# Kernel optimization log

Hardware: AMD Instinct MI355X
Metric: run time of the kernel (lower is better)

## Reference

```python
import jax, jax.numpy as jnp
import numpy as np
from functools import partial

DIM = 256
HEADS = 8
HEAD_DIM = DIM // HEADS
SCALES = (1, 2, 4)
B, H, W = 1, 64, 64


def _dwconv3x3(x, w, b):
    # x: (B,C,H,W), w: (C,1,3,3) depthwise, b: (C,)
    y = jax.lax.conv_general_dilated(
        x, w, window_strides=(1, 1), padding='SAME',
        feature_group_count=x.shape[1],
        dimension_numbers=('NCHW', 'OIHW', 'NCHW'))
    return y + b[None, :, None, None]


def _pwconv(x, w, b):
    # 1x1 conv: x (B,C,H,W), w (O,C), b (O,)
    return jnp.einsum('bchw,oc->bohw', x, w) + b[None, :, None, None]


def _avg_pool(x, s):
    Bb, C, Hh, Ww = x.shape
    return x.reshape(Bb, C, Hh // s, s, Ww // s, s).mean(axis=(3, 5))


def setup_inputs() -> dict:
    key = jax.random.key(0)
    ks = jax.random.split(key, 9)
    sc = 0.05
    return {
        'x': jax.random.normal(ks[0], (B, DIM, H, W), dtype=jnp.float32),
        'dw_w': jax.random.normal(ks[1], (3, DIM, 1, 3, 3), dtype=jnp.float32) * sc,
        'dw_b': jax.random.normal(ks[2], (3, DIM), dtype=jnp.float32) * sc,
        'pw_w': jax.random.normal(ks[3], (3, 3 * DIM, DIM), dtype=jnp.float32) * sc,
        'pw_b': jax.random.normal(ks[4], (3, 3 * DIM), dtype=jnp.float32) * sc,
        'pos_w': jax.random.normal(ks[5], (3, DIM, 1, 3, 3), dtype=jnp.float32) * sc,
        'pos_b': jax.random.normal(ks[6], (3, DIM), dtype=jnp.float32) * sc,
        'fusion_w': jax.random.normal(ks[7], (DIM, 3 * DIM), dtype=jnp.float32) * sc,
        'fusion_b': jax.random.normal(ks[8], (DIM,), dtype=jnp.float32) * sc,
    }


def reference(x, dw_w, dw_b, pw_w, pw_b, pos_w, pos_b, fusion_w, fusion_b):
    Bb, C, Hh, Ww = x.shape
    outputs = []
    for i, scale in enumerate(SCALES):
        xs = _avg_pool(x, scale) if scale > 1 else x
        # ConvQKV
        x_dw = _dwconv3x3(xs, dw_w[i], dw_b[i])
        qkv = _pwconv(x_dw, pw_w[i], pw_b[i])
        q, k, v = jnp.split(qkv, 3, axis=1)
        pos = _dwconv3x3(xs, pos_w[i], pos_b[i])
        q = q + pos
        k = k + pos
        Hs, Ws = xs.shape[2], xs.shape[3]
        Ns = Hs * Ws
        # (B, heads, head_dim, N)
        q = q.reshape(Bb, HEADS, HEAD_DIM, Ns)
        k = k.reshape(Bb, HEADS, HEAD_DIM, Ns)
        v = v.reshape(Bb, HEADS, HEAD_DIM, Ns)
        attn = jnp.einsum('bhdn,bhdm->bhnm', q, k) / (HEAD_DIM ** 0.5)
        attn = jax.nn.softmax(attn, axis=-1)
        out = jnp.einsum('bhnm,bhdm->bhdn', attn, v)  # (B,h,hd,N)
        out = out.reshape(Bb, C, Hs, Ws)
        if scale > 1:
            out = jax.image.resize(out, (Bb, C, Hh, Ww), method='bilinear')
        outputs.append(out)
    cat = jnp.concatenate(outputs, axis=1)  # (B, 3C, H, W)
    return jnp.einsum('bchw,oc->bohw', cat, fusion_w) + fusion_b[None, :, None, None]
```

## Files before the change

### kernel.cpp

```cpp
#include <hip/hip_runtime.h>
#include <math.h>

#define DIM 256
#define HEADS 8
#define HD 32
#define QSCALE 0.25504526770295183f

typedef __attribute__((ext_vector_type(8))) short bf16x8;
typedef __attribute__((ext_vector_type(4))) float f32x4;

#if __has_builtin(__builtin_amdgcn_exp2f)
#define EXP2(x) __builtin_amdgcn_exp2f(x)
#else
#define EXP2(x) __expf((x) * 0.6931471805599453f)
#endif

__device__ __forceinline__ unsigned short f2bf(float f) {
  unsigned int u = __float_as_uint(f);
  unsigned int r = u + 0x7fff + ((u >> 16) & 1);
  return (unsigned short)(r >> 16);
}
__device__ __forceinline__ float bf2f(unsigned short u) {
  return __uint_as_float(((unsigned int)u) << 16);
}


__global__ __launch_bounds__(256) void prep_kernel(const float* __restrict__ x,
    const float* __restrict__ pw_w, const float* __restrict__ fus_w,
    float* __restrict__ xs2, float* __restrict__ xs4,
    unsigned short* __restrict__ Wb, unsigned short* __restrict__ Wf) {
  const int gx = blockIdx.x, t = threadIdx.x;
  if (gx < 1024) {
    int id = gx * 256 + t;
    int c = id >> 10, n = id & 1023;
    int y = (n >> 5) << 1, x0 = (n & 31) << 1;
    const float* b = x + c * 4096 + y * 64 + x0;
    xs2[id] = (b[0] + b[1] + b[64] + b[65]) * 0.25f;
  } else if (gx < 1280) {
    int id = (gx - 1024) * 256 + t;
    int c = id >> 8, n = id & 255;
    int y = (n >> 4) << 2, x0 = (n & 15) << 2;
    const float* b = x + c * 4096 + y * 64 + x0;
    float s = 0.f;
    #pragma unroll
    for (int dy = 0; dy < 4; ++dy)
      #pragma unroll
      for (int dx = 0; dx < 4; ++dx) s += b[dy * 64 + dx];
    xs4[id] = s * 0.0625f;
  } else if (gx < 1424) {
    int lid = (gx - 1280) * 256 + t;
    int fb = lid >> 5, l = lid & 31;
    int scale = fb / 384, bs = fb - scale * 384;
    int rtile = bs >> 3, kchunk = bs & 7;
    int r = scale * 768 + rtile * 16 + (l & 7) * 2;
    int k = kchunk * 32 + (l >> 3) * 8;
    const float* s0 = pw_w + (size_t)r * 256 + k;
    float4 u0 = *(const float4*)(s0);
    float4 u1 = *(const float4*)(s0 + 4);
    float4 u2 = *(const float4*)(s0 + 256);
    float4 u3 = *(const float4*)(s0 + 260);
    unsigned short* d = Wb + (size_t)fb * 512 + l * 16;
    ushort4 a0 = {f2bf(u0.x), f2bf(u0.y), f2bf(u0.z), f2bf(u0.w)};
    ushort4 a1 = {f2bf(u1.x), f2bf(u1.y), f2bf(u1.z), f2bf(u1.w)};
    ushort4 a2 = {f2bf(u2.x), f2bf(u2.y), f2bf(u2.z), f2bf(u2.w)};
    ushort4 a3 = {f2bf(u3.x), f2bf(u3.y), f2bf(u3.z), f2bf(u3.w)};
    *(ushort4*)(d)      = a0;
    *(ushort4*)(d + 4)  = a1;
    *(ushort4*)(d + 8)  = a2;
    *(ushort4*)(d + 12) = a3;
  } else {
    int lid = (gx - 1424) * 256 + t;
    int fb = lid >> 5, l = lid & 31;
    int rtile = fb / 24, kchunk = fb - rtile * 24;
    int r = rtile * 16 + (l & 7) * 2;
    int k = kchunk * 32 + (l >> 3) * 8;
    const float* s0 = fus_w + (size_t)r * 768 + k;
    float4 u0 = *(const float4*)(s0);
    float4 u1 = *(const float4*)(s0 + 4);
    float4 u2 = *(const float4*)(s0 + 768);
    float4 u3 = *(const float4*)(s0 + 772);
    unsigned short* d = Wf + (size_t)fb * 512 + l * 16;
    ushort4 a0 = {f2bf(u0.x), f2bf(u0.y), f2bf(u0.z), f2bf(u0.w)};
    ushort4 a1 = {f2bf(u1.x), f2bf(u1.y), f2bf(u1.z), f2bf(u1.w)};
    ushort4 a2 = {f2bf(u2.x), f2bf(u2.y), f2bf(u2.z), f2bf(u2.w)};
    ushort4 a3 = {f2bf(u3.x), f2bf(u3.y), f2bf(u3.z), f2bf(u3.w)};
    *(ushort4*)(d)      = a0;
    *(ushort4*)(d + 4)  = a1;
    *(ushort4*)(d + 8)  = a2;
    *(ushort4*)(d + 12) = a3;
  }
}

__global__ __launch_bounds__(256) void dwt_kernel(const float* __restrict__ x,
    const float* __restrict__ xs2, const float* __restrict__ xs4,
    const float* __restrict__ dw_w, const float* __restrict__ dw_b,
    const float* __restrict__ pos_w, const float* __restrict__ pos_b,
    unsigned short* __restrict__ xdwT, unsigned short* __restrict__ posT) {
  __shared__ unsigned short lds1[32][72];
  __shared__ unsigned short lds2[32][72];
  int b = blockIdx.x;
  const float* src;
  int lgHs, wo, soff;
  if (b < 512)      { src = x;   lgHs = 6; wo = 0; soff = 0; }
  else if (b < 640) { b -= 512; src = xs2; lgHs = 5; wo = 1; soff = 1048576; }
  else              { b -= 640; src = xs4; lgHs = 4; wo = 2; soff = 1310720; }
  const int c0 = (b & 3) * 64;
  const int n0 = (b >> 2) * 32;
  const int Hs = 1 << lgHs;
  const int Ns = Hs * Hs;
  const int t = threadIdx.x;
  #pragma unroll
  for (int p = 0; p < 2; ++p) {
    int cl = p * 32 + (t >> 3);
    int c = c0 + cl;
    const float* w1 = dw_w + wo * 2304 + c * 9;
    const float* w2 = pos_w + wo * 2304 + c * 9;
    float b1 = dw_b[wo * 256 + c], b2 = pos_b[wo * 256 + c];
    int nb = (t & 7) * 4;
    int gn = n0 + nb;
    int y = gn >> lgHs, xg = gn & (Hs - 1);
    const float* sc = src + c * Ns;
    float r[3][6];
    #pragma unroll
    for (int ky = 0; ky < 3; ++ky) {
      int yy = y + ky - 1;
      bool rok = (yy >= 0) && (yy < Hs);
      #pragma unroll
      for (int j = 0; j < 6; ++j) {
        int xx = xg - 1 + j;
        r[ky][j] = (rok && xx >= 0 && xx < Hs) ? sc[yy * Hs + xx] : 0.f;
      }
    }
    #pragma unroll
    for (int i = 0; i < 4; ++i) {
      float s1 = b1, s2 = b2;
      #pragma unroll
      for (int ky = 0; ky < 3; ++ky)
        #pragma unroll
        for (int kx = 0; kx < 3; ++kx) {
          float v = r[ky][i + kx];
          s1 += v * w1[ky * 3 + kx];
          s2 += v * w2[ky * 3 + kx];
        }
      lds1[nb + i][cl] = f2bf(s1);
      lds2[nb + i][cl] = f2bf(s2);
    }
  }
  __syncthreads();
  {
    int blk = t >> 6, l = t & 63;
    int ntile = blk >> 1, cchunk = blk & 1;
    int koct = l >> 4, rr = l & 15;
    size_t bid = (size_t)((n0 >> 4) + ntile) * 8 + (c0 >> 5) + cchunk;
    *(bf16x8*)(xdwT + soff + bid * 512 + (size_t)l * 8) =
        *(const bf16x8*)&lds1[ntile * 16 + rr][cchunk * 32 + koct * 8];
  }
  {
    int n = t >> 3, cseg = (t & 7) * 8;
    *(bf16x8*)(posT + soff + (size_t)(n0 + n) * 256 + c0 + cseg) =
        *(const bf16x8*)&lds2[n][cseg];
  }
}

__global__ __launch_bounds__(256) void gemm_qkv_all(const unsigned short* __restrict__ WbA,
    const unsigned short* __restrict__ xdwTA, const float* __restrict__ biasA,
    const unsigned short* __restrict__ posTA, unsigned short* __restrict__ Qf,
    unsigned short* __restrict__ Kf, unsigned short* __restrict__ Vf) {
  int by = blockIdx.y;
  int Ns, off;
  const unsigned short *Wb, *xdwT, *posT;
  const float* bias;
  if (by < 64) {
    Ns = 4096; off = 0;
    Wb = WbA; bias = biasA;
  } else if (by < 80) {
    Ns = 1024; off = 1048576; by -= 64;
    Wb = WbA + 196608; bias = biasA + 768;
  } else {
    Ns = 256; off = 1310720; by -= 80;
    Wb = WbA + 393216; bias = biasA + 1536;
  }
  xdwT = xdwTA + off; posT = posTA + off;
  const int t = threadIdx.x;
  const int wave = t >> 6, lane = t & 63;
  const int ln = lane & 15, quad = lane >> 4;
  const int o0 = blockIdx.x * 64 + (wave & 1) * 32;
  const int n0 = by * 64 + (wave >> 1) * 32;
  const int at0 = (o0 >> 4) * 8, at1 = at0 + 8;
  const int bt0 = (n0 >> 4) * 8, bt1 = bt0 + 8;
  const bool vblk = blockIdx.x >= 8;
  f32x4 acc[2][2] = {};
  if (!vblk) {
    #pragma unroll
    for (int ks = 0; ks < 8; ++ks) {
      bf16x8 af0 = *(const bf16x8*)(Wb + (size_t)(at0 + ks) * 512 + lane * 8);
      bf16x8 af1 = *(const bf16x8*)(Wb + (size_t)(at1 + ks) * 512 + lane * 8);
      bf16x8 bv0 = *(const bf16x8*)(xdwT + (size_t)(bt0 + ks) * 512 + lane * 8);
      bf16x8 bv1 = *(const bf16x8*)(xdwT + (size_t)(bt1 + ks) * 512 + lane * 8);
      acc[0][0] = __builtin_amdgcn_mfma_f32_16x16x32_bf16(af0, bv0, acc[0][0], 0, 0, 0);
      acc[0][1] = __builtin_amdgcn_mfma_f32_16x16x32_bf16(af0, bv1, acc[0][1], 0, 0, 0);
      acc[1][0] = __builtin_amdgcn_mfma_f32_16x16x32_bf16(af1, bv0, acc[1][0], 0, 0, 0);
      acc[1][1] = __builtin_amdgcn_mfma_f32_16x16x32_bf16(af1, bv1, acc[1][1], 0, 0, 0);
    }
  } else {
    #pragma unroll
    for (int ks = 0; ks < 8; ++ks) {
      bf16x8 af0 = *(const bf16x8*)(Wb + (size_t)(at0 + ks) * 512 + lane * 8);
      bf16x8 af1 = *(const bf16x8*)(Wb + (size_t)(at1 + ks) * 512 + lane * 8);
      bf16x8 bv0 = *(const bf16x8*)(xdwT + (size_t)(bt0 + ks) * 512 + lane * 8);
      bf16x8 bv1 = *(const bf16x8*)(xdwT + (size_t)(bt1 + ks) * 512 + lane * 8);
      acc[0][0] = __builtin_amdgcn_mfma_f32_16x16x32_bf16(bv0, af0, acc[0][0], 0, 0, 0);
      acc[0][1] = __builtin_amdgcn_mfma_f32_16x16x32_bf16(bv0, af1, acc[0][1], 0, 0, 0);
      acc[1][0] = __builtin_amdgcn_mfma_f32_16x16x32_bf16(bv1, af0, acc[1][0], 0, 0, 0);
      acc[1][1] = __builtin_amdgcn_mfma_f32_16x16x32_bf16(bv1, af1, acc[1][1], 0, 0, 0);
    }
  }
  if (!vblk) {
    const int cat = blockIdx.x >> 2;
    #pragma unroll
    for (int mt = 0; mt < 2; ++mt) {
      int ot = o0 + mt * 16 + quad * 4;
      float bs0 = bias[ot], bs1 = bias[ot + 1], bs2 = bias[ot + 2], bs3 = bias[ot + 3];
      #pragma unroll
      for (int nt = 0; nt < 2; ++nt) {
        int nn = n0 + nt * 16 + ln;
        f32x4 v = acc[mt][nt];
        v.x += bs0; v.y += bs1; v.z += bs2; v.w += bs3;
        int c = ot & 255;
        ushort4 p4 = *(const ushort4*)(posT + (size_t)nn * 256 + c);
        v.x += bf2f(p4.x); v.y += bf2f(p4.y); v.z += bf2f(p4.z); v.w += bf2f(p4.w);
        if (cat == 0) { v.x *= QSCALE; v.y *= QSCALE; v.z *= QSCALE; v.w *= QSCALE; }
        ushort4 st;
        st.x = f2bf(v.x); st.y = f2bf(v.y); st.z = f2bf(v.z); st.w = f2bf(v.w);
        int hh = c >> 5, d = c & 31;
        unsigned short* dst = (cat == 0 ? Qf : Kf) + off;
        size_t a = ((size_t)(hh * (Ns >> 4) + (nn >> 4)) * 64 + (d >> 3) * 16 + (nn & 15)) * 8
                   + (d & 7);
        *(ushort4*)(dst + a) = st;
      }
    }
  } else {
    #pragma unroll
    for (int a = 0; a < 2; ++a) {
      int nbase = n0 + a * 16 + quad * 4;
      #pragma unroll
      for (int bb = 0; bb < 2; ++bb) {
        int o = o0 + bb * 16 + ln;
        int c = o - 512;
        int hh = c >> 5, d = c & 31;
        int dt = d >> 4, dl = d & 15;
        float bs = bias[o];
        f32x4 v = acc[a][bb];
        ushort4 st;
        st.x = f2bf(v.x + bs); st.y = f2bf(v.y + bs);
        st.z = f2bf(v.z + bs); st.w = f2bf(v.w + bs);
        size_t adr = ((((size_t)hh * (Ns >> 5) + (nbase >> 5)) * 2 + dt) * 64
                      + ((nbase & 31) >> 3) * 16 + dl) * 8 + (nbase & 7);
        *(ushort4*)(Vf + off + adr) = st;
      }
    }
  }
}

__global__ __launch_bounds__(256) void attn_all_kernel(
    const unsigned short* __restrict__ Qf, const unsigned short* __restrict__ Kf,
    const unsigned short* __restrict__ Vf,
    unsigned short* __restrict__ accp1, unsigned short* __restrict__ p2,
    unsigned short* __restrict__ p4, float* __restrict__ ls1,
    float* __restrict__ ls2, float* __restrict__ ls4) {
  __shared__ unsigned short pt_lds[4 * 32 * 72];
  const int z = blockIdx.z;
  unsigned short* accp;
  float* lsump;
  int Ns, lgMs, sp, off;
  if (z < 8) {
    accp = accp1; lsump = ls1; Ns = 4096; lgMs = 9; sp = z; off = 0;
  } else if (z < 16) {
    if (blockIdx.x >= 8) return;
    accp = p2; lsump = ls2; Ns = 1024; lgMs = 7; sp = z - 8; off = 1048576;
  } else {
    if (blockIdx.x >= 2) return;
    accp = p4; lsump = ls4; Ns = 256; lgMs = 6; sp = z - 16; off = 1310720;
  }
  const int t = threadIdx.x;
  const int wave = t >> 6, lane = t & 63;
  const int ln = lane & 15, quad = lane >> 4;
  const int h = blockIdx.y;
  const int n0 = blockIdx.x * 128 + wave * 32;
  const unsigned short* qp = Qf + off
      + ((size_t)(h * (Ns >> 4) + (n0 >> 4)) * 64 + lane) * 8;
  bf16x8 qf0 = *(const bf16x8*)(qp);
  bf16x8 qf1 = *(const bf16x8*)(qp + 512);
  unsigned short* ptw = pt_lds + wave * (32 * 72);
  f32x4 acc[2][2] = {};
  f32x4 acc_l0 = {0.f, 0.f, 0.f, 0.f}, acc_l1 = {0.f, 0.f, 0.f, 0.f};
  const f32x4 zero = {0.f, 0.f, 0.f, 0.f};
  const short kOne = (short)0x3F80;
  const bf16x8 onesf = {kOne, kOne, kOne, kOne, kOne, kOne, kOne, kOne};
  const int m0s = sp << lgMs;
  const int nch = 1 << (lgMs - 6);
  const unsigned short* kp = Kf + off
      + ((size_t)(h * (Ns >> 4) + (m0s >> 4)) * 64 + lane) * 8;
  const unsigned short* vp = Vf + off
      + (((size_t)h * (Ns >> 5) + (m0s >> 5)) * 128 + lane) * 8;
  for (int ch = 0; ch < nch; ++ch) {
    const unsigned short* kc = kp + ch * 2048;
    const unsigned short* vc = vp + ch * 2048;
    bf16x8 kf0 = *(const bf16x8*)(kc);
    bf16x8 kf1 = *(const bf16x8*)(kc + 512);
    bf16x8 kf2 = *(const bf16x8*)(kc + 1024);
    bf16x8 kf3 = *(const bf16x8*)(kc + 1536);
    bf16x8 vf00 = *(const bf16x8*)(vc);
    bf16x8 vf10 = *(const bf16x8*)(vc + 512);
    bf16x8 vf01 = *(const bf16x8*)(vc + 1024);
    bf16x8 vf11 = *(const bf16x8*)(vc + 1536);
    f32x4 s[4][2];
    s[0][0] = __builtin_amdgcn_mfma_f32_16x16x32_bf16(kf0, qf0, zero, 0, 0, 0);
    s[0][1] = __builtin_amdgcn_mfma_f32_16x16x32_bf16(kf0, qf1, zero, 0, 0, 0);
    s[1][0] = __builtin_amdgcn_mfma_f32_16x16x32_bf16(kf1, qf0, zero, 0, 0, 0);
    s[1][1] = __builtin_amdgcn_mfma_f32_16x16x32_bf16(kf1, qf1, zero, 0, 0, 0);
    s[2][0] = __builtin_amdgcn_mfma_f32_16x16x32_bf16(kf2, qf0, zero, 0, 0, 0);
    s[2][1] = __builtin_amdgcn_mfma_f32_16x16x32_bf16(kf2, qf1, zero, 0, 0, 0);
    s[3][0] = __builtin_amdgcn_mfma_f32_16x16x32_bf16(kf3, qf0, zero, 0, 0, 0);
    s[3][1] = __builtin_amdgcn_mfma_f32_16x16x32_bf16(kf3, qf1, zero, 0, 0, 0);
    #pragma unroll
    for (int mt = 0; mt < 4; ++mt) {
      #pragma unroll
      for (int nt = 0; nt < 2; ++nt) {
        float e0 = EXP2(s[mt][nt].x);
        float e1 = EXP2(s[mt][nt].y);
        float e2 = EXP2(s[mt][nt].z);
        float e3 = EXP2(s[mt][nt].w);
        uint2 pk;
        pk.x = __builtin_amdgcn_perm(__float_as_uint(e1), __float_as_uint(e0), 0x07060302);
        pk.y = __builtin_amdgcn_perm(__float_as_uint(e3), __float_as_uint(e2), 0x07060302);
        *(uint2*)&ptw[(nt * 16 + ln) * 72 + mt * 16 + quad * 4] = pk;
      }
    }
    #pragma unroll
    for (int ks = 0; ks < 2; ++ks) {
      bf16x8 pf0 = *(const bf16x8*)&ptw[ln * 72 + ks * 32 + quad * 8];
      bf16x8 pf1 = *(const bf16x8*)&ptw[(16 + ln) * 72 + ks * 32 + quad * 8];
      bf16x8 va = ks ? vf01 : vf00;
      bf16x8 vbf = ks ? vf11 : vf10;
      acc[0][0] = __builtin_amdgcn_mfma_f32_16x16x32_bf16(va, pf0, acc[0][0], 0, 0, 0);
      acc[0][1] = __builtin_amdgcn_mfma_f32_16x16x32_bf16(va, pf1, acc[0][1], 0, 0, 0);
      acc[1][0] = __builtin_amdgcn_mfma_f32_16x16x32_bf16(vbf, pf0, acc[1][0], 0, 0, 0);
      acc[1][1] = __builtin_amdgcn_mfma_f32_16x16x32_bf16(vbf, pf1, acc[1][1], 0, 0, 0);
      acc_l0 = __builtin_amdgcn_mfma_f32_16x16x32_bf16(onesf, pf0, acc_l0, 0, 0, 0);
      acc_l1 = __builtin_amdgcn_mfma_f32_16x16x32_bf16(onesf, pf1, acc_l1, 0, 0, 0);
    }
  }
  unsigned short* ap = accp + ((size_t)sp * 256 + h * 32) * Ns;
  #pragma unroll
  for (int dt = 0; dt < 2; ++dt) {
    #pragma unroll
    for (int r = 0; r < 4; ++r) {
      int cl = dt * 16 + quad * 4 + r;
      ap[(size_t)cl * Ns + n0 + ln]      = f2bf(((const float*)&acc[dt][0])[r]);
      ap[(size_t)cl * Ns + n0 + 16 + ln] = f2bf(((const float*)&acc[dt][1])[r]);
    }
  }
  if (lane < 16) {
    float* lp = lsump + ((size_t)sp * 8 + h) * Ns + n0;
    lp[lane]      = acc_l0.x;
    lp[16 + lane] = acc_l1.x;
  }
}

__global__ __launch_bounds__(256) void combine24_kernel(const unsigned short* __restrict__ p2,
    const float* __restrict__ ls2, const unsigned short* __restrict__ p4,
    const float* __restrict__ ls4, float* __restrict__ out2, float* __restrict__ out4) {
  int id = blockIdx.x * 256 + threadIdx.x;
  if (id < 262144) {
    int n = id & 1023, h = id >> 15;
    float v = 0.f, d = 0.f;
    #pragma unroll
    for (int sp = 0; sp < 8; ++sp) {
      v += bf2f(p2[sp * 262144 + id]);
      d += ls2[sp * 8192 + h * 1024 + n];
    }
    out2[id] = v / d;
  } else {
    int idl = id - 262144;
    int n = idl & 255, h = idl >> 13;
    float v = 0.f, d = 0.f;
    #pragma unroll
    for (int sp = 0; sp < 4; ++sp) {
      v += bf2f(p4[sp * 65536 + idl]);
      d += ls4[sp * 2048 + h * 256 + n];
    }
    out4[idl] = v / d;
  }
}

__global__ __launch_bounds__(256) void build_catT_kernel(const unsigned short* __restrict__ accp,
    const float* __restrict__ lsum1, const float* __restrict__ out2,
    const float* __restrict__ out4, unsigned short* __restrict__ catT) {
  __shared__ unsigned short lds[64][72];
  const int t = threadIdx.x;
  const int n0 = blockIdx.x * 64;
  const int by = blockIdx.y;
  const int c0 = by * 64;
  if (by < 4) {
    #pragma unroll
    for (int p = 0; p < 4; ++p) {
      int ct = p * 16 + (t >> 4);
      int c = c0 + ct;
      int h = c >> 5;
      int nn = (t & 15) * 4;
      float vs[4] = {0.f, 0.f, 0.f, 0.f};
      float ds[4] = {0.f, 0.f, 0.f, 0.f};
      #pragma unroll
      for (int sp = 0; sp < 8; ++sp) {
        ushort4 a = *(const ushort4*)(accp + (size_t)sp * 1048576 + (size_t)c * 4096 + n0 + nn);
        vs[0] += bf2f(a.x); vs[1] += bf2f(a.y); vs[2] += bf2f(a.z); vs[3] += bf2f(a.w);
        float4 dd = *(const float4*)(lsum1 + (size_t)sp * 32768 + (size_t)h * 4096 + n0 + nn);
        ds[0] += dd.x; ds[1] += dd.y; ds[2] += dd.z; ds[3] += dd.w;
      }
      lds[nn + 0][ct] = f2bf(vs[0] / ds[0]);
      lds[nn + 1][ct] = f2bf(vs[1] / ds[1]);
      lds[nn + 2][ct] = f2bf(vs[2] / ds[2]);
      lds[nn + 3][ct] = f2bf(vs[3] / ds[3]);
    }
  } else {
    const bool s2 = by < 8;
    const float* src = s2 ? out2 : out4;
    const int Hs = s2 ? 32 : 16;
    const int coff = s2 ? 256 : 512;
    const float sc = (float)Hs / 64.0f;
    #pragma unroll
    for (int p = 0; p < 4; ++p) {
      int ct = p * 16 + (t >> 4);
      const float* s = src + (size_t)(c0 - coff + ct) * Hs * Hs;
      int nn = (t & 15) * 4;
      #pragma unroll
      for (int i = 0; i < 4; ++i) {
        int n = n0 + nn + i;
        int y = n >> 6, x = n & 63;
        float fy = ((float)y + 0.5f) * sc - 0.5f;
        float fx = ((float)x + 0.5f) * sc - 0.5f;
        float fy0 = floorf(fy), fx0 = floorf(fx);
        int y0 = (int)fy0, x0 = (int)fx0;
        float ty = fy - fy0, tx = fx - fx0;
        int y0c = min(max(y0, 0), Hs - 1), y1c = min(max(y0 + 1, 0), Hs - 1);
        int x0c = min(max(x0, 0), Hs - 1), x1c = min(max(x0 + 1, 0), Hs - 1);
        float v00 = s[y0c * Hs + x0c], v01 = s[y0c * Hs + x1c];
        float v10 = s[y1c * Hs + x0c], v11 = s[y1c * Hs + x1c];
        float v0 = v00 + (v01 - v00) * tx;
        float v1 = v10 + (v11 - v10) * tx;
        lds[nn + i][ct] = f2bf(v0 + (v1 - v0) * ty);
      }
    }
  }
  __syncthreads();
  int blk = t >> 5, l = t & 31;
  int ntile = blk >> 1, cchunk = blk & 1;
  int koct = l >> 3, r1 = (l & 7) * 2;
  size_t bid = (size_t)((n0 >> 4) + ntile) * 24 + (c0 >> 5) + cchunk;
  unsigned short* dst = catT + bid * 512 + (size_t)l * 16;
  *(bf16x8*)(dst)     = *(const bf16x8*)&lds[ntile * 16 + r1][cchunk * 32 + koct * 8];
  *(bf16x8*)(dst + 8) = *(const bf16x8*)&lds[ntile * 16 + r1 + 1][cchunk * 32 + koct * 8];
}

__global__ __launch_bounds__(256) void gemm_fus_mfma(const unsigned short* __restrict__ Wf,
    const unsigned short* __restrict__ catT, float* __restrict__ part) {
  const int t = threadIdx.x;
  const int wave = t >> 6, lane = t & 63;
  const int ln = lane & 15, quad = lane >> 4;
  const int o0 = blockIdx.x * 64 + (wave & 1) * 32;
  const int n0 = blockIdx.y * 64 + (wave >> 1) * 32;
  const int sp = blockIdx.z;
  const int at0 = (o0 >> 4) * 24 + sp * 8, at1 = at0 + 24;
  const int bt0 = (n0 >> 4) * 24 + sp * 8, bt1 = bt0 + 24;
  f32x4 acc[2][2] = {};
  #pragma unroll
  for (int ks = 0; ks < 8; ++ks) {
    bf16x8 af0 = *(const bf16x8*)(Wf + (size_t)(at0 + ks) * 512 + lane * 8);
    bf16x8 af1 = *(const bf16x8*)(Wf + (size_t)(at1 + ks) * 512 + lane * 8);
    bf16x8 bv0 = *(const bf16x8*)(catT + (size_t)(bt0 + ks) * 512 + lane * 8);
    bf16x8 bv1 = *(const bf16x8*)(catT + (size_t)(bt1 + ks) * 512 + lane * 8);
    acc[0][0] = __builtin_amdgcn_mfma_f32_16x16x32_bf16(bv0, af0, acc[0][0], 0, 0, 0);
    acc[0][1] = __builtin_amdgcn_mfma_f32_16x16x32_bf16(bv0, af1, acc[0][1], 0, 0, 0);
    acc[1][0] = __builtin_amdgcn_mfma_f32_16x16x32_bf16(bv1, af0, acc[1][0], 0, 0, 0);
    acc[1][1] = __builtin_amdgcn_mfma_f32_16x16x32_bf16(bv1, af1, acc[1][1], 0, 0, 0);
  }
  float* pp = part + (size_t)sp * 1048576;
  #pragma unroll
  for (int a = 0; a < 2; ++a) {
    int nbase = n0 + a * 16 + quad * 4;
    #pragma unroll
    for (int bb = 0; bb < 2; ++bb) {
      int o = o0 + bb * 16 + ln;
      float4 st;
      st.x = acc[a][bb].x; st.y = acc[a][bb].y; st.z = acc[a][bb].z; st.w = acc[a][bb].w;
      *(float4*)(pp + (size_t)o * 4096 + nbase) = st;
    }
  }
}

__global__ __launch_bounds__(256) void fus_combine_kernel(const float* __restrict__ part,
    const float* __restrict__ bias, float* __restrict__ out) {
  int id = blockIdx.x * 256 + threadIdx.x;
  int o = id >> 10;
  float4 v0 = *(const float4*)(part + id * 4);
  float4 v1 = *(const float4*)(part + 1048576 + id * 4);
  float4 v2 = *(const float4*)(part + 2097152 + id * 4);
  float bs = bias[o];
  float4 r;
  r.x = v0.x + v1.x + v2.x + bs;
  r.y = v0.y + v1.y + v2.y + bs;
  r.z = v0.z + v1.z + v2.z + bs;
  r.w = v0.w + v1.w + v2.w + bs;
  *(float4*)(out + id * 4) = r;
}

extern "C" void kernel_launch(void* const* d_in, const int* in_sizes, int n_in,
                              void* d_out, int out_size, void* d_ws, size_t ws_size,
                              hipStream_t stream) {
  const float* x     = (const float*)d_in[0];
  const float* dw_w  = (const float*)d_in[1];
  const float* dw_b  = (const float*)d_in[2];
  const float* pw_w  = (const float*)d_in[3];
  const float* pw_b  = (const float*)d_in[4];
  const float* pos_w = (const float*)d_in[5];
  const float* pos_b = (const float*)d_in[6];
  const float* fus_w = (const float*)d_in[7];
  const float* fus_b = (const float*)d_in[8];
  float* out = (float*)d_out;
  float* ws = (float*)d_ws;

  float* scratch = ws;
  float* posF   = ws + 1376256;
  float* accpF  = ws + 2752512;
  unsigned short* xdwT = (unsigned short*)(ws + 6946816);
  unsigned short* posT = (unsigned short*)(ws + 7634944);
  unsigned short* Qf   = (unsigned short*)(ws + 8323072);
  unsigned short* Kf   = Qf + 1376256;
  unsigned short* Vf   = (unsigned short*)(ws + 9699328);
  unsigned short* catT = (unsigned short*)(ws + 10387456);
  unsigned short* Wf   = (unsigned short*)(ws + 11960320);

  float* xs2 = accpF;
  float* xs4 = accpF + 262144;
  unsigned short* Wb = catT;
  unsigned short* accp = (unsigned short*)accpF;
  float* lsump1 = posF;
  float* lsump2 = posF + 262144;
  float* lsump4 = posF + 327680;
  float* out2   = posF + 335872;
  float* out4   = posF + 598016;
  unsigned short* p2 = (unsigned short*)scratch;
  unsigned short* p4 = (unsigned short*)scratch + 2097152;
  float* part = accpF;

  prep_kernel<<<1472, 256, 0, stream>>>(x, pw_w, fus_w, xs2, xs4, Wb, Wf);
  dwt_kernel<<<672, 256, 0, stream>>>(x, xs2, xs4, dw_w, dw_b, pos_w, pos_b, xdwT, posT);
  gemm_qkv_all<<<dim3(12, 84), 256, 0, stream>>>(Wb, xdwT, pw_b, posT, Qf, Kf, Vf);

  attn_all_kernel<<<dim3(32, 8, 20), 256, 0, stream>>>(Qf, Kf, Vf, accp, p2, p4,
                                                       lsump1, lsump2, lsump4);
  combine24_kernel<<<1280, 256, 0, stream>>>(p2, lsump2, p4, lsump4, out2, out4);

  build_catT_kernel<<<dim3(64, 12), 256, 0, stream>>>(accp, lsump1, out2, out4, catT);
  gemm_fus_mfma<<<dim3(4, 64, 3), 256, 0, stream>>>(Wf, catT, part);
  fus_combine_kernel<<<1024, 256, 0, stream>>>(part, fus_b, out);
}
```

Baseline: 150.7 us.

## Stage K/V chunks through double-buffered LDS shared across waves

```diff
diff --git a/kernel.cpp b/kernel.cpp
--- a/kernel.cpp
+++ b/kernel.cpp
@@ -269,6 +269,7 @@
     unsigned short* __restrict__ p4, float* __restrict__ ls1,
     float* __restrict__ ls2, float* __restrict__ ls4) {
   __shared__ unsigned short pt_lds[4 * 32 * 72];
+  __shared__ unsigned short kvbuf[2][4096];
   const int z = blockIdx.z;
   unsigned short* accp;
   float* lsump;
@@ -299,21 +300,29 @@
   const bf16x8 onesf = {kOne, kOne, kOne, kOne, kOne, kOne, kOne, kOne};
   const int m0s = sp << lgMs;
   const int nch = 1 << (lgMs - 6);
-  const unsigned short* kp = Kf + off
-      + ((size_t)(h * (Ns >> 4) + (m0s >> 4)) * 64 + lane) * 8;
-  const unsigned short* vp = Vf + off
-      + (((size_t)h * (Ns >> 5) + (m0s >> 5)) * 128 + lane) * 8;
+  const unsigned short* kg = Kf + off + ((size_t)(h * (Ns >> 4) + (m0s >> 4))) * 512;
+  const unsigned short* vg = Vf + off + ((size_t)(h * (Ns >> 5) + (m0s >> 5)) * 2) * 512;
+  *(bf16x8*)&kvbuf[0][t * 8]        = *(const bf16x8*)(kg + (size_t)t * 8);
+  *(bf16x8*)&kvbuf[0][2048 + t * 8] = *(const bf16x8*)(vg + (size_t)t * 8);
+  __syncthreads();
+  int cur = 0;
   for (int ch = 0; ch < nch; ++ch) {
-    const unsigned short* kc = kp + ch * 2048;
-    const unsigned short* vc = vp + ch * 2048;
-    bf16x8 kf0 = *(const bf16x8*)(kc);
-    bf16x8 kf1 = *(const bf16x8*)(kc + 512);
-    bf16x8 kf2 = *(const bf16x8*)(kc + 1024);
-    bf16x8 kf3 = *(const bf16x8*)(kc + 1536);
-    bf16x8 vf00 = *(const bf16x8*)(vc);
-    bf16x8 vf10 = *(const bf16x8*)(vc + 512);
-    bf16x8 vf01 = *(const bf16x8*)(vc + 1024);
-    bf16x8 vf11 = *(const bf16x8*)(vc + 1536);
+    if (ch + 1 < nch) {
+      *(bf16x8*)&kvbuf[cur ^ 1][t * 8] =
+          *(const bf16x8*)(kg + (size_t)(ch + 1) * 2048 + t * 8);
+      *(bf16x8*)&kvbuf[cur ^ 1][2048 + t * 8] =
+          *(const bf16x8*)(vg + (size_t)(ch + 1) * 2048 + t * 8);
+    }
+    const unsigned short* kb = &kvbuf[cur][lane * 8];
+    const unsigned short* vb = &kvbuf[cur][2048 + lane * 8];
+    bf16x8 kf0 = *(const bf16x8*)(kb);
+    bf16x8 kf1 = *(const bf16x8*)(kb + 512);
+    bf16x8 kf2 = *(const bf16x8*)(kb + 1024);
+    bf16x8 kf3 = *(const bf16x8*)(kb + 1536);
+    bf16x8 vf00 = *(const bf16x8*)(vb);
+    bf16x8 vf10 = *(const bf16x8*)(vb + 512);
+    bf16x8 vf01 = *(const bf16x8*)(vb + 1024);
+    bf16x8 vf11 = *(const bf16x8*)(vb + 1536);
     f32x4 s[4][2];
     s[0][0] = __builtin_amdgcn_mfma_f32_16x16x32_bf16(kf0, qf0, zero, 0, 0, 0);
     s[0][1] = __builtin_amdgcn_mfma_f32_16x16x32_bf16(kf0, qf1, zero, 0, 0, 0);
@@ -350,6 +359,8 @@
       acc_l0 = __builtin_amdgcn_mfma_f32_16x16x32_bf16(onesf, pf0, acc_l0, 0, 0, 0);
       acc_l1 = __builtin_amdgcn_mfma_f32_16x16x32_bf16(onesf, pf1, acc_l1, 0, 0, 0);
     }
+    __syncthreads();
+    cur ^= 1;
   }
   unsigned short* ap = accp + ((size_t)sp * 256 + h * 32) * Ns;
   #pragma unroll
```

After: 152.5 us. About the same (+1.2%).

## Replace fusion split-K partial buffer with atomic accumulation and relayout pos tensor

Applied to the files above, without the earlier changes.

```diff
diff --git a/kernel.cpp b/kernel.cpp
--- a/kernel.cpp
+++ b/kernel.cpp
@@ -28,7 +28,8 @@
 __global__ __launch_bounds__(256) void prep_kernel(const float* __restrict__ x,
     const float* __restrict__ pw_w, const float* __restrict__ fus_w,
     float* __restrict__ xs2, float* __restrict__ xs4,
-    unsigned short* __restrict__ Wb, unsigned short* __restrict__ Wf) {
+    unsigned short* __restrict__ Wb, unsigned short* __restrict__ Wf,
+    float* __restrict__ out) {
   const int gx = blockIdx.x, t = threadIdx.x;
   if (gx < 1024) {
     int id = gx * 256 + t;
@@ -68,7 +69,7 @@
     *(ushort4*)(d + 4)  = a1;
     *(ushort4*)(d + 8)  = a2;
     *(ushort4*)(d + 12) = a3;
-  } else {
+  } else if (gx < 1472) {
     int lid = (gx - 1424) * 256 + t;
     int fb = lid >> 5, l = lid & 31;
     int rtile = fb / 24, kchunk = fb - rtile * 24;
@@ -88,6 +89,14 @@
     *(ushort4*)(d + 4)  = a1;
     *(ushort4*)(d + 8)  = a2;
     *(ushort4*)(d + 12) = a3;
+  } else {
+    int id = (gx - 1472) * 256 + t;
+    float4 z = {0.f, 0.f, 0.f, 0.f};
+    float* p = out + (size_t)id * 16;
+    *(float4*)(p)      = z;
+    *(float4*)(p + 4)  = z;
+    *(float4*)(p + 8)  = z;
+    *(float4*)(p + 12) = z;
   }
 }
 
@@ -95,70 +104,62 @@
     const float* __restrict__ xs2, const float* __restrict__ xs4,
     const float* __restrict__ dw_w, const float* __restrict__ dw_b,
     const float* __restrict__ pos_w, const float* __restrict__ pos_b,
-    unsigned short* __restrict__ xdwT, unsigned short* __restrict__ posT) {
-  __shared__ unsigned short lds1[32][72];
-  __shared__ unsigned short lds2[32][72];
+    unsigned short* __restrict__ xdwT, unsigned short* __restrict__ posTc) {
+  __shared__ __align__(16) unsigned short lds1[32][40];
   int b = blockIdx.x;
   const float* src;
   int lgHs, wo, soff;
-  if (b < 512)      { src = x;   lgHs = 6; wo = 0; soff = 0; }
-  else if (b < 640) { b -= 512; src = xs2; lgHs = 5; wo = 1; soff = 1048576; }
-  else              { b -= 640; src = xs4; lgHs = 4; wo = 2; soff = 1310720; }
-  const int c0 = (b & 3) * 64;
-  const int n0 = (b >> 2) * 32;
+  if (b < 1024)      { src = x;   lgHs = 6; wo = 0; soff = 0; }
+  else if (b < 1280) { b -= 1024; src = xs2; lgHs = 5; wo = 1; soff = 1048576; }
+  else               { b -= 1280; src = xs4; lgHs = 4; wo = 2; soff = 1310720; }
+  const int c0 = (b & 7) * 32;
+  const int n0 = (b >> 3) * 32;
   const int Hs = 1 << lgHs;
   const int Ns = Hs * Hs;
   const int t = threadIdx.x;
+  const int cl = t >> 3;
+  const int c = c0 + cl;
+  const int nb = (t & 7) * 4;
+  const float* w1 = dw_w + wo * 2304 + c * 9;
+  const float* w2 = pos_w + wo * 2304 + c * 9;
+  const float b1 = dw_b[wo * 256 + c], b2 = pos_b[wo * 256 + c];
+  const int gn = n0 + nb;
+  const int y = gn >> lgHs, xg = gn & (Hs - 1);
+  const float* sc = src + c * Ns;
+  float r[3][6];
   #pragma unroll
-  for (int p = 0; p < 2; ++p) {
-    int cl = p * 32 + (t >> 3);
-    int c = c0 + cl;
-    const float* w1 = dw_w + wo * 2304 + c * 9;
-    const float* w2 = pos_w + wo * 2304 + c * 9;
-    float b1 = dw_b[wo * 256 + c], b2 = pos_b[wo * 256 + c];
-    int nb = (t & 7) * 4;
-    int gn = n0 + nb;
-    int y = gn >> lgHs, xg = gn & (Hs - 1);
-    const float* sc = src + c * Ns;
-    float r[3][6];
-    #pragma unroll
-    for (int ky = 0; ky < 3; ++ky) {
-      int yy = y + ky - 1;
-      bool rok = (yy >= 0) && (yy < Hs);
-      #pragma unroll
-      for (int j = 0; j < 6; ++j) {
-        int xx = xg - 1 + j;
-        r[ky][j] = (rok && xx >= 0 && xx < Hs) ? sc[yy * Hs + xx] : 0.f;
+  for (int ky = 0; ky < 3; ++ky) {
+    int yy = y + ky - 1;
+    bool rok = (yy >= 0) && (yy < Hs);
+    #pragma unroll
+    for (int j = 0; j < 6; ++j) {
+      int xx = xg - 1 + j;
+      r[ky][j] = (rok && xx >= 0 && xx < Hs) ? sc[yy * Hs + xx] : 0.f;
+    }
+  }
+  ushort4 pst;
+  unsigned short* ps = (unsigned short*)&pst;
+  #pragma unroll
+  for (int i = 0; i < 4; ++i) {
+    float s1 = b1, s2 = b2;
+    #pragma unroll
+    for (int ky = 0; ky < 3; ++ky)
+      #pragma unroll
+      for (int kx = 0; kx < 3; ++kx) {
+        float v = r[ky][i + kx];
+        s1 += v * w1[ky * 3 + kx];
+        s2 += v * w2[ky * 3 + kx];
       }
-    }
-    #pragma unroll
-    for (int i = 0; i < 4; ++i) {
-      float s1 = b1, s2 = b2;
-      #pragma unroll
-      for (int ky = 0; ky < 3; ++ky)
-        #pragma unroll
-        for (int kx = 0; kx < 3; ++kx) {
-          float v = r[ky][i + kx];
-          s1 += v * w1[ky * 3 + kx];
-          s2 += v * w2[ky * 3 + kx];
-        }
-      lds1[nb + i][cl] = f2bf(s1);
-      lds2[nb + i][cl] = f2bf(s2);
-    }
-  }
+    lds1[nb + i][cl] = f2bf(s1);
+    ps[i] = f2bf(s2);
+  }
+  *(ushort4*)(posTc + soff + (size_t)c * Ns + gn) = pst;
   __syncthreads();
-  {
+  if (t < 128) {
     int blk = t >> 6, l = t & 63;
-    int ntile = blk >> 1, cchunk = blk & 1;
-    int koct = l >> 4, rr = l & 15;
-    size_t bid = (size_t)((n0 >> 4) + ntile) * 8 + (c0 >> 5) + cchunk;
+    size_t bid = (size_t)((n0 >> 4) + blk) * 8 + (c0 >> 5);
     *(bf16x8*)(xdwT + soff + bid * 512 + (size_t)l * 8) =
-        *(const bf16x8*)&lds1[ntile * 16 + rr][cchunk * 32 + koct * 8];
-  }
-  {
-    int n = t >> 3, cseg = (t & 7) * 8;
-    *(bf16x8*)(posT + soff + (size_t)(n0 + n) * 256 + c0 + cseg) =
-        *(const bf16x8*)&lds2[n][cseg];
+        *(const bf16x8*)&lds1[blk * 16 + (l & 15)][(l >> 4) * 8];
   }
 }
 
@@ -221,18 +222,20 @@
     for (int mt = 0; mt < 2; ++mt) {
       int ot = o0 + mt * 16 + quad * 4;
       float bs0 = bias[ot], bs1 = bias[ot + 1], bs2 = bias[ot + 2], bs3 = bias[ot + 3];
+      int cb = ot & 255;
       #pragma unroll
       for (int nt = 0; nt < 2; ++nt) {
         int nn = n0 + nt * 16 + ln;
         f32x4 v = acc[mt][nt];
-        v.x += bs0; v.y += bs1; v.z += bs2; v.w += bs3;
-        int c = ot & 255;
-        ushort4 p4 = *(const ushort4*)(posT + (size_t)nn * 256 + c);
-        v.x += bf2f(p4.x); v.y += bf2f(p4.y); v.z += bf2f(p4.z); v.w += bf2f(p4.w);
+        const unsigned short* pp = posT + (size_t)cb * Ns + nn;
+        v.x += bs0 + bf2f(pp[0]);
+        v.y += bs1 + bf2f(pp[Ns]);
+        v.z += bs2 + bf2f(pp[2 * Ns]);
+        v.w += bs3 + bf2f(pp[3 * Ns]);
         if (cat == 0) { v.x *= QSCALE; v.y *= QSCALE; v.z *= QSCALE; v.w *= QSCALE; }
         ushort4 st;
         st.x = f2bf(v.x); st.y = f2bf(v.y); st.z = f2bf(v.z); st.w = f2bf(v.w);
-        int hh = c >> 5, d = c & 31;
+        int hh = cb >> 5, d = cb & 31;
         unsigned short* dst = (cat == 0 ? Qf : Kf) + off;
         size_t a = ((size_t)(hh * (Ns >> 4) + (nn >> 4)) * 64 + (d >> 3) * 16 + (nn & 15)) * 8
                    + (d & 7);
@@ -464,7 +467,8 @@
 }
 
 __global__ __launch_bounds__(256) void gemm_fus_mfma(const unsigned short* __restrict__ Wf,
-    const unsigned short* __restrict__ catT, float* __restrict__ part) {
+    const unsigned short* __restrict__ catT, const float* __restrict__ bias,
+    float* __restrict__ out) {
   const int t = threadIdx.x;
   const int wave = t >> 6, lane = t & 63;
   const int ln = lane & 15, quad = lane >> 4;
@@ -485,34 +489,20 @@
     acc[1][0] = __builtin_amdgcn_mfma_f32_16x16x32_bf16(bv1, af0, acc[1][0], 0, 0, 0);
     acc[1][1] = __builtin_amdgcn_mfma_f32_16x16x32_bf16(bv1, af1, acc[1][1], 0, 0, 0);
   }
-  float* pp = part + (size_t)sp * 1048576;
   #pragma unroll
   for (int a = 0; a < 2; ++a) {
     int nbase = n0 + a * 16 + quad * 4;
     #pragma unroll
     for (int bb = 0; bb < 2; ++bb) {
       int o = o0 + bb * 16 + ln;
-      float4 st;
-      st.x = acc[a][bb].x; st.y = acc[a][bb].y; st.z = acc[a][bb].z; st.w = acc[a][bb].w;
-      *(float4*)(pp + (size_t)o * 4096 + nbase) = st;
-    }
-  }
-}
-
-__global__ __launch_bounds__(256) void fus_combine_kernel(const float* __restrict__ part,
-    const float* __restrict__ bias, float* __restrict__ out) {
-  int id = blockIdx.x * 256 + threadIdx.x;
-  int o = id >> 10;
-  float4 v0 = *(const float4*)(part + id * 4);
-  float4 v1 = *(const float4*)(part + 1048576 + id * 4);
-  float4 v2 = *(const float4*)(part + 2097152 + id * 4);
-  float bs = bias[o];
-  float4 r;
-  r.x = v0.x + v1.x + v2.x + bs;
-  r.y = v0.y + v1.y + v2.y + bs;
-  r.z = v0.z + v1.z + v2.z + bs;
-  r.w = v0.w + v1.w + v2.w + bs;
-  *(float4*)(out + id * 4) = r;
+      float badd = (sp == 0) ? bias[o] : 0.f;
+      float* po = out + (size_t)o * 4096 + nbase;
+      atomicAdd(po + 0, acc[a][bb].x + badd);
+      atomicAdd(po + 1, acc[a][bb].y + badd);
+      atomicAdd(po + 2, acc[a][bb].z + badd);
+      atomicAdd(po + 3, acc[a][bb].w + badd);
+    }
+  }
 }
 
 extern "C" void kernel_launch(void* const* d_in, const int* in_sizes, int n_in,
@@ -534,7 +524,7 @@
   float* posF   = ws + 1376256;
   float* accpF  = ws + 2752512;
   unsigned short* xdwT = (unsigned short*)(ws + 6946816);
-  unsigned short* posT = (unsigned short*)(ws + 7634944);
+  unsigned short* posTc = (unsigned short*)(ws + 7634944);
   unsigned short* Qf   = (unsigned short*)(ws + 8323072);
   unsigned short* Kf   = Qf + 1376256;
   unsigned short* Vf   = (unsigned short*)(ws + 9699328);
@@ -552,17 +542,15 @@
   float* out4   = posF + 598016;
   unsigned short* p2 = (unsigned short*)scratch;
   unsigned short* p4 = (unsigned short*)scratch + 2097152;
-  float* part = accpF;
-
-  prep_kernel<<<1472, 256, 0, stream>>>(x, pw_w, fus_w, xs2, xs4, Wb, Wf);
-  dwt_kernel<<<672, 256, 0, stream>>>(x, xs2, xs4, dw_w, dw_b, pos_w, pos_b, xdwT, posT);
-  gemm_qkv_all<<<dim3(12, 84), 256, 0, stream>>>(Wb, xdwT, pw_b, posT, Qf, Kf, Vf);
+
+  prep_kernel<<<1728, 256, 0, stream>>>(x, pw_w, fus_w, xs2, xs4, Wb, Wf, out);
+  dwt_kernel<<<1344, 256, 0, stream>>>(x, xs2, xs4, dw_w, dw_b, pos_w, pos_b, xdwT, posTc);
+  gemm_qkv_all<<<dim3(12, 84), 256, 0, stream>>>(Wb, xdwT, pw_b, posTc, Qf, Kf, Vf);
 
   attn_all_kernel<<<dim3(32, 8, 20), 256, 0, stream>>>(Qf, Kf, Vf, accp, p2, p4,
                                                        lsump1, lsump2, lsump4);
   combine24_kernel<<<1280, 256, 0, stream>>>(p2, lsump2, p4, lsump4, out2, out4);
 
   build_catT_kernel<<<dim3(64, 12), 256, 0, stream>>>(accp, lsump1, out2, out4, catT);
-  gemm_fus_mfma<<<dim3(4, 64, 3), 256, 0, stream>>>(Wf, catT, part);
-  fus_combine_kernel<<<1024, 256, 0, stream>>>(part, fus_b, out);
-}
+  gemm_fus_mfma<<<dim3(4, 64, 3), 256, 0, stream>>>(Wf, catT, fus_b, out);
+}
```

After: 183.1 us. +21.5%, slower.
